# Performance work log

Hardware: AMD Instinct MI355X
Metric: run time of the kernel (lower is better)

Reference implementation:

```python
import jax, jax.numpy as jnp
import numpy as np

B, NPTS = 2, 60000
NX, NY = 256, 256
PCR0, PCR1 = -32.0, -32.0
PS0, PS1 = 0.25, 0.25
MAXPP = 32      # max points per pillar
MAXP = 12000    # max pillars
C = 64          # lidar_channels
SENT = NX * NY  # sentinel pillar id (> any valid id)
NEG = -1e9
EPS = 1e-5


def setup_inputs():
    key = jax.random.key(0)
    ks = jax.random.split(key, 16)
    xy = jax.random.uniform(ks[0], (B, NPTS, 2), minval=-34.0, maxval=34.0)
    z = jax.random.uniform(ks[1], (B, NPTS, 1), minval=-3.0, maxval=1.0)
    ir = jax.random.uniform(ks[2], (B, NPTS, 2))
    pts = jnp.concatenate([xy, z, ir], axis=-1).astype(jnp.float32)
    mask = jax.random.uniform(ks[3], (B, NPTS)) < 0.98

    def lin(k, i, o):
        return (jax.random.normal(k, (i, o)) / np.sqrt(i)).astype(jnp.float32)

    inp = {"lidar_points": pts, "lidar_mask": mask,
           "w1": lin(ks[4], 10, 64), "b1": 0.01 * jax.random.normal(ks[5], (64,), jnp.float32),
           "g1": jnp.ones(64, jnp.float32), "be1": jnp.zeros(64, jnp.float32),
           "w2": lin(ks[6], 64, 64), "b2": 0.01 * jax.random.normal(ks[7], (64,), jnp.float32),
           "g2": jnp.ones(64, jnp.float32), "be2": jnp.zeros(64, jnp.float32)}
    for i, n in enumerate(["1", "2", "3"]):
        inp["cw" + n] = (jax.random.normal(ks[8 + i], (64, 64, 3, 3)) / np.sqrt(64 * 9)).astype(jnp.float32)
        inp["cb" + n] = 0.01 * jax.random.normal(ks[11 + i], (64,), jnp.float32)
        inp["cg" + n] = jnp.ones(64, jnp.float32)
        inp["cbe" + n] = jnp.zeros(64, jnp.float32)
    return inp


def bn1d(x, g, b):  # training-mode BN over rows (biased var), matches torch BatchNorm1d forward
    m = x.mean(0)
    v = ((x - m) ** 2).mean(0)
    return (x - m) * jax.lax.rsqrt(v + EPS) * g + b


def bn2d(x, g, b):  # training-mode BN over (N,H,W) per channel
    m = x.mean((0, 2, 3), keepdims=True)
    v = ((x - m) ** 2).mean((0, 2, 3), keepdims=True)
    return (x - m) * jax.lax.rsqrt(v + EPS) * g[None, :, None, None] + b[None, :, None, None]


def conv3(x, w, b):
    y = jax.lax.conv_general_dilated(x, w, (1, 1), 'SAME',
                                     dimension_numbers=('NCHW', 'OIHW', 'NCHW'))
    return y + b[None, :, None, None]


def pillarize(pts, msk):
    """pts: (N,5) xyzir, msk: (N,) bool -> padded pillar tensors (fixed shapes)."""
    n = pts.shape[0]
    ix = jnp.clip(((pts[:, 0] - PCR0) / PS0).astype(jnp.int32), 0, NX - 1)
    iy = jnp.clip(((pts[:, 1] - PCR1) / PS1).astype(jnp.int32), 0, NY - 1)
    pid = jnp.where(msk, iy * NX + ix, SENT)
    # sorted unique ids; keep the first (smallest) MAXP, like torch.unique + truncation
    spid = jnp.sort(pid)
    is_new = jnp.concatenate([jnp.array([True]), spid[1:] != spid[:-1]])
    urank = jnp.cumsum(is_new) - 1
    dest = jnp.where(is_new & (urank < MAXP) & (spid < SENT), urank, MAXP)
    uids = jnp.full((MAXP + 1,), SENT, dtype=pid.dtype).at[dest].set(spid)[:MAXP]  # ascending, SENT-padded
    inv = jnp.clip(jnp.searchsorted(uids, pid), 0, MAXP - 1)
    valid = (uids[inv] == pid) & (pid < SENT)
    # rank of each point within its pillar, in original point order (stable sort)
    seg = jnp.where(valid, inv, MAXP)
    order = jnp.argsort(seg)  # stable
    sseg = seg[order]
    pos = jnp.arange(n)
    first = jnp.concatenate([jnp.array([True]), sseg[1:] != sseg[:-1]])
    start = jax.lax.cummax(jnp.where(first, pos, 0))
    rank = jnp.zeros(n, jnp.int32).at[order].set((pos - start).astype(jnp.int32))
    keep = valid & (rank < MAXPP)  # first MAXPP points per pillar (matches truncation-then-mean)
    seg2 = jnp.where(keep, inv, MAXP)  # dump slot = MAXP
    cnt = jnp.zeros(MAXP + 1, pts.dtype).at[seg2].add(1.0)
    sums = jnp.zeros((MAXP + 1, 3), pts.dtype).at[seg2].add(jnp.where(keep[:, None], pts[:, :3], 0.0))
    mean = sums / jnp.maximum(cnt, 1.0)[:, None]
    ctr = mean[seg2]  # per-point pillar centroid (over kept points)
    gx = PCR0 + ((pid % NX).astype(pts.dtype) + 0.5) * PS0
    gy = PCR1 + ((pid // NX).astype(pts.dtype) + 0.5) * PS1
    aug = jnp.concatenate([pts, pts[:, :3] - ctr, gx[:, None], gy[:, None]], axis=1)  # (N,10)
    rk = jnp.minimum(rank, MAXPP - 1)
    pf = jnp.zeros((MAXP + 1, MAXPP, 10), pts.dtype).at[seg2, rk].set(
        jnp.where(keep[:, None], aug, 0.0))[:MAXP]
    pm = jnp.zeros((MAXP + 1, MAXPP), bool).at[seg2, rk].set(keep)[:MAXP]
    pvalid = uids < SENT
    coords = jnp.where(pvalid[:, None], jnp.stack([uids % NX, uids // NX], axis=-1), 0)
    return pf, pm, coords, pvalid


def pillar_net(pf, pm, w1, b1, g1, be1, w2, b2, g2, be2):
    npil, pp, ci = pf.shape
    x = pf.reshape(npil * pp, ci) @ w1 + b1
    x = jax.nn.relu(bn1d(x, g1, be1))
    x = x @ w2 + b2
    x = jax.nn.relu(bn1d(x, g2, be2))
    x = x.reshape(npil, pp, -1)
    x = jnp.where(pm[:, :, None], x, NEG)
    return x.max(axis=1)  # (npil, C)


def reference(lidar_points, lidar_mask, w1, b1, g1, be1, w2, b2, g2, be2,
              cw1, cb1, cg1, cbe1, cw2, cb2, cg2, cbe2, cw3, cb3, cg3, cbe3):
    pf, pm, coords, pvalid = jax.vmap(pillarize)(lidar_points, lidar_mask)
    # pillar net is applied per batch element in the original loop -> per-sample BN stats
    feat = jax.vmap(lambda a, m: pillar_net(a, m, w1, b1, g1, be1, w2, b2, g2, be2))(pf, pm)
    lin = coords[..., 1] * NX + coords[..., 0]          # (B, MAXP)
    f = jnp.where(pvalid[..., None], feat, 0.0)          # padded pillars contribute nothing
    bev = jax.vmap(lambda l, ff: jnp.zeros((NY * NX, C), ff.dtype).at[l].add(ff))(lin, f)
    bev = bev.reshape(-1, NY, NX, C).transpose(0, 3, 1, 2)  # (B,C,NY,NX)
    x = jax.nn.relu(bn2d(conv3(bev, cw1, cb1), cg1, cbe1))
    x = jax.nn.relu(bn2d(conv3(x, cw2, cb2), cg2, cbe2))
    x = jax.nn.relu(bn2d(conv3(x, cw3, cb3), cg3, cbe3))
    return x
```

## Files before the change

kernel.cpp:

```cpp
#include <hip/hip_runtime.h>

#define NPTS 60000
#define NXG 256
#define NCELL 65536
#define MAXP 12000
#define MAXPP 32
#define NROWS (MAXP*MAXPP)

typedef float f32x32 __attribute__((ext_vector_type(32)));
typedef float f32x4  __attribute__((ext_vector_type(4)));
typedef short s16x8  __attribute__((ext_vector_type(8)));

__device__ __forceinline__ short to_bf16(float f){
  unsigned u = __float_as_uint(f);
  unsigned r = (u + 0x7FFFu + ((u>>16)&1u)) >> 16;
  return (short)r;
}

__global__ __launch_bounds__(256) void zero_bufs(uint4* __restrict__ p1, size_t n1,
                                                 uint4* __restrict__ p2, size_t n2){
  size_t idx = (size_t)blockIdx.x*256 + threadIdx.x;
  size_t stride = (size_t)gridDim.x*256;
  const uint4 z = make_uint4(0,0,0,0);
  for (size_t k=idx; k<n1; k+=stride) p1[k]=z;
  for (size_t k=idx; k<n2; k+=stride) p2[k]=z;
}

__global__ void compute_pid(const float* __restrict__ pts, const void* __restrict__ maskp,
                            int* __restrict__ pid, int* __restrict__ pptr,
                            int* __restrict__ ccnt){
  __shared__ int cf32, cbig;
  if (threadIdx.x==0){ cf32=0; cbig=0; }
  __syncthreads();
  {
    int lf=0, lb=0;
    const unsigned* mu = (const unsigned*)maskp;
    for (int k=0;k<4;k++){
      unsigned x = mu[threadIdx.x*4+k];
      if (x==0x3f800000u) lf++;
      else if (x>1u) lb++;
    }
    if (lf) atomicAdd(&cf32, lf);
    if (lb) atomicAdd(&cbig, lb);
  }
  __syncthreads();
  int mode = (cf32>64) ? 2 : ((cbig>0) ? 1 : 0);
  int i = blockIdx.x*blockDim.x + threadIdx.x;
  if (i>=NPTS) return;
  int b = blockIdx.y;
  int gi = b*NPTS+i;
  bool m;
  if (mode==0)      m = ((const int*)maskp)[gi]!=0;
  else if (mode==1) m = ((const unsigned char*)maskp)[gi]!=0;
  else              m = ((const float*)maskp)[gi]!=0.f;
  int cell = -1;
  if (m){
    float x = pts[(size_t)gi*5+0], y = pts[(size_t)gi*5+1];
    int ix = (int)((x - (-32.0f)) / 0.25f);
    ix = ix<0?0:(ix>255?255:ix);
    int iy = (int)((y - (-32.0f)) / 0.25f);
    iy = iy<0?0:(iy>255?255:iy);
    cell = iy*NXG + ix;
    atomicAdd(&ccnt[b*NCELL+cell], 1);
  }
  pid[gi] = cell;
  pptr[gi] = -1;
}

__global__ __launch_bounds__(256) void scan_a(const int* __restrict__ ccnt,
                                              int2* __restrict__ bpart){
  int b = blockIdx.y, blk = blockIdx.x, t = threadIdx.x;
  int4 v = *(const int4*)&ccnt[b*NCELL + blk*1024 + t*4];
  int occ = (v.x>0)+(v.y>0)+(v.z>0)+(v.w>0);
  int cnt = v.x+v.y+v.z+v.w;
  #pragma unroll
  for (int off=32; off>0; off>>=1){
    occ += __shfl_xor(occ, off, 64);
    cnt += __shfl_xor(cnt, off, 64);
  }
  __shared__ int so[4], sc[4];
  int wv = t>>6, lane = t&63;
  if (lane==0){ so[wv]=occ; sc[wv]=cnt; }
  __syncthreads();
  if (t==0) bpart[b*64+blk] = make_int2(so[0]+so[1]+so[2]+so[3], sc[0]+sc[1]+sc[2]+sc[3]);
}

__global__ __launch_bounds__(256) void scan_b(const int* __restrict__ ccnt,
    const int2* __restrict__ bpart,
    int* __restrict__ crank, int* __restrict__ cstart, int* __restrict__ pcell,
    int* __restrict__ misc, int* __restrict__ heavy){
  __shared__ int swo[4], swc[4], sk[4];
  __shared__ int bo_, bc_;
  int b = blockIdx.y, blk = blockIdx.x, t = threadIdx.x;
  int wv = t>>6, lane = t&63;
  if (t < 64){
    int2 p = bpart[b*64+t];
    int po = (t<blk)? p.x : 0;
    int pc = (t<blk)? p.y : 0;
    int to = p.x;
    int tc = p.y;
    #pragma unroll
    for (int off=32; off>0; off>>=1){
      po += __shfl_xor(po, off, 64);
      pc += __shfl_xor(pc, off, 64);
      to += __shfl_xor(to, off, 64);
      tc += __shfl_xor(tc, off, 64);
    }
    if (t==0){
      bo_ = po; bc_ = pc;
      if (blk==0){
        misc[1+b] = (to < MAXP) ? to : MAXP;
        misc[5+b] = tc;
      }
    }
  }
  int4 v = *(const int4*)&ccnt[b*NCELL + blk*1024 + t*4];
  int occ = (v.x>0)+(v.y>0)+(v.z>0)+(v.w>0);
  int cnt = v.x+v.y+v.z+v.w;
  int io = occ, ic = cnt;
  #pragma unroll
  for (int off=1; off<64; off<<=1){
    int ao = __shfl_up(io, off, 64);
    int ac = __shfl_up(ic, off, 64);
    if (lane >= off){ io += ao; ic += ac; }
  }
  if (lane==63){ swo[wv]=io; swc[wv]=ic; }
  __syncthreads();
  int wvo=0, wvc=0;
  #pragma unroll
  for (int w2=0; w2<4; w2++){
    if (w2<wv){ wvo += swo[w2]; wvc += swc[w2]; }
  }
  int eo = bo_ + wvo + io - occ;
  int ec = bc_ + wvc + ic - cnt;
  int kept = 0;
  int cellb = blk*1024 + t*4;
  int vv[4] = {v.x,v.y,v.z,v.w};
  #pragma unroll
  for (int j=0;j<4;j++){
    int c = cellb+j; int val = vv[j];
    if (val>0){
      crank[b*NCELL+c]=eo; cstart[b*NCELL+c]=ec;
      if (eo<MAXP){
        pcell[b*MAXP+eo]=c;
        kept += (val<MAXPP)? val : MAXPP;
        if (val>MAXPP){
          int hi = atomicAdd(&heavy[b],1);
          if (hi<64) heavy[2 + b*64 + hi] = c;
        }
      }
      eo++; ec+=val;
    }
  }
  #pragma unroll
  for (int off=32; off>0; off>>=1) kept += __shfl_xor(kept, off, 64);
  if (lane==0) sk[wv]=kept;
  __syncthreads();
  if (t==0) atomicAdd(&misc[3+b], sk[0]+sk[1]+sk[2]+sk[3]);
}

__global__ void scatter_points(const int* __restrict__ pid, const int* __restrict__ ccnt,
    const int* __restrict__ crank, const int* __restrict__ cstart,
    int* __restrict__ ctmp, int* __restrict__ plist, int* __restrict__ pptr){
  int i = blockIdx.x*blockDim.x + threadIdx.x;
  if (i>=NPTS) return;
  int b = blockIdx.y;
  int gi = b*NPTS+i;
  int cell = pid[gi];
  if (cell<0) return;
  int bc = b*NCELL+cell;
  int pos = cstart[bc] + atomicAdd(&ctmp[bc],1);
  plist[b*NPTS+pos] = i;
  int r = crank[bc];
  if (r>=0 && r<MAXP && ccnt[bc]<=MAXPP) pptr[gi] = r;
}

__global__ void heavy_select(const int* __restrict__ ccnt, const int* __restrict__ crank,
    const int* __restrict__ cstart, const int* __restrict__ plist,
    const int* __restrict__ heavy, int* __restrict__ pptr){
  int b = blockIdx.y;
  int hn = heavy[b]; if (hn>64) hn=64;
  if ((int)blockIdx.x >= hn) return;
  int cell = heavy[2 + b*64 + blockIdx.x];
  int bc = b*NCELL+cell;
  int cnt = ccnt[bc], start = cstart[bc], pr = crank[bc];
  for (int e=threadIdx.x; e<cnt; e+=blockDim.x){
    int pe = plist[b*NPTS+start+e];
    int rank=0;
    for (int k=0;k<cnt;k++) rank += (plist[b*NPTS+start+k] < pe);
    if (rank<MAXPP) pptr[b*NPTS+pe] = pr;
  }
}

__global__ __launch_bounds__(256) void gather_cpts(const float* __restrict__ pts,
    const int* __restrict__ pid, const int* __restrict__ pptr,
    const int* __restrict__ plist, const int* __restrict__ misc,
    float* __restrict__ cpts, float* __restrict__ psum){
  int pos = blockIdx.x*256 + threadIdx.x;
  int b = blockIdx.y;
  if (pos >= misc[5+b]) return;
  int i = plist[b*NPTS+pos];
  int gi = b*NPTS+i;
  const float* qp = &pts[(size_t)gi*5];
  float x=qp[0], y=qp[1], z=qp[2], i1=qp[3], i2=qp[4];
  int cell = pid[gi];
  int rid = pptr[gi];
  float gx = -32.0f + ((float)(cell&255)+0.5f)*0.25f;
  float gy = -32.0f + ((float)(cell>>8)+0.5f)*0.25f;
  float4* cp = (float4*)&cpts[(size_t)(b*NPTS+pos)*8];
  cp[0] = make_float4(x,y,z,i1);
  cp[1] = make_float4(i2,gx,gy,__int_as_float(rid));
  if (rid>=0){
    float* s = &psum[(size_t)(b*MAXP+rid)*4];
    atomicAdd(s+0,x); atomicAdd(s+1,y); atomicAdd(s+2,z); atomicAdd(s+3,1.f);
  }
}

#define MM_ACC(K,V) { if ((K)<32) m0[(K)&31]+=(V); else if ((K)<64) m1[((K)-32)&31]+=(V); else m2+=(V); }
__global__ __launch_bounds__(256) void moments(const float* __restrict__ cpts,
    const float* __restrict__ psum, const int* __restrict__ misc,
    float* __restrict__ lstat){
  int b = blockIdx.y;
  int n = misc[5+b];
  f32x32 m0, m1; float m2 = 0.f;
  #pragma unroll
  for (int j=0;j<32;j++){ m0[j]=0.f; m1[j]=0.f; }
  for (int pos = blockIdx.x*256+threadIdx.x; pos<n; pos += gridDim.x*256){
    const float4* cp = (const float4*)&cpts[(size_t)(b*NPTS+pos)*8];
    float4 f1 = cp[0], f2 = cp[1];
    int rid = __float_as_int(f2.w);
    if (rid<0) continue;
    float4 mc = *(const float4*)&psum[(size_t)(b*MAXP+rid)*4];
    float inv = 1.f/fmaxf(mc.w,1.f);
    float aug[10] = {f1.x,f1.y,f1.z,f1.w,f2.x,
                     f1.x-mc.x*inv, f1.y-mc.y*inv, f1.z-mc.z*inv, f2.y, f2.z};
    #pragma unroll
    for (int d=0; d<10; d++){
      #pragma unroll
      for (int e=d; e<10; e++){
        const int k = d*10 - d*(d-1)/2 + (e-d);
        MM_ACC(k, aug[d]*aug[e]);
      }
      const int kl = 55+d;
      MM_ACC(kl, aug[d]);
    }
  }
  int lane = threadIdx.x & 63;
  int rep = ((blockIdx.x*256+threadIdx.x)>>6) & 15;
  float* dst = &lstat[(size_t)(rep*2+b)*65];
  #pragma unroll
  for (int j=0;j<32;j++){
    float v = m0[j];
    #pragma unroll
    for (int off=32; off>0; off>>=1) v += __shfl_xor(v, off, 64);
    if (lane==0) atomicAdd(&dst[j], v);
  }
  #pragma unroll
  for (int j=0;j<32;j++){
    float v = m1[j];
    #pragma unroll
    for (int off=32; off>0; off>>=1) v += __shfl_xor(v, off, 64);
    if (lane==0) atomicAdd(&dst[32+j], v);
  }
  {
    float v = m2;
    #pragma unroll
    for (int off=32; off>0; off>>=1) v += __shfl_xor(v, off, 64);
    if (lane==0) atomicAdd(&dst[64], v);
  }
}

__global__ void stats_fin1(const float* __restrict__ w1, const float* __restrict__ b1,
    const float* __restrict__ g1, const float* __restrict__ be1,
    const float* __restrict__ w2, const float* __restrict__ b2,
    const float* __restrict__ lstat, float* __restrict__ stats,
    const int* __restrict__ misc){
  __shared__ float M[65];
  __shared__ float z0s[64];
  int b = blockIdx.x, c = threadIdx.x;
  for (int e=c; e<65; e+=64){
    float s=0.f;
    for (int r=0;r<16;r++) s += lstat[(size_t)(r*2+b)*65+e];
    M[e]=s;
  }
  __syncthreads();
  float* S = &stats[(size_t)b*512];
  float wcol[10];
  #pragma unroll
  for (int d=0;d<10;d++) wcol[d] = w1[d*64+c];
  float b1c = b1[c];
  float nk = (float)misc[3+b];
  const float N = (float)NROWS;
  float pad = N - nk;
  float lw = 0.f;
  #pragma unroll
  for (int d=0;d<10;d++) lw += M[55+d]*wcol[d];
  float s = nk*b1c + lw;
  float qq = nk*b1c*b1c + 2.f*b1c*lw;
  #pragma unroll
  for (int d=0; d<10; d++){
    #pragma unroll
    for (int e=d; e<10; e++){
      float m = M[d*10 - d*(d-1)/2 + (e-d)];
      qq += ((d==e)?1.f:2.f)*m*wcol[d]*wcol[e];
    }
  }
  float St = s + pad*b1c;
  float Qt = qq + pad*b1c*b1c;
  float mu = St/N;
  float var = fmaxf(Qt/N - mu*mu, 0.f);
  float sc = g1[c]*rsqrtf(var+1e-5f);
  float sh = be1[c]-mu*sc;
  S[256+c]=sc; S[320+c]=sh;
  float z0 = fmaxf(b1c*sc+sh, 0.f);
  z0s[c]=z0;
  __syncthreads();
  float t0 = b2[c];
  for (int i2=0;i2<64;i2++) t0 += z0s[i2]*w2[(size_t)i2*64+c];
  S[128+c]=pad*t0; S[192+c]=pad*t0*t0;
}

__global__ __launch_bounds__(256) void pillar_mlp(const float* __restrict__ cpts,
    const int* __restrict__ pcell, const int* __restrict__ cstart,
    const int* __restrict__ ccnt, const float* __restrict__ psum,
    const int* __restrict__ misc,
    const float* __restrict__ w1, const float* __restrict__ b1,
    const float* __restrict__ w2, const float* __restrict__ b2,
    const float* __restrict__ stats, float* __restrict__ l2stat,
    float* __restrict__ fmx, float* __restrict__ fmn){
  const int lane = threadIdx.x & 63;
  float w1c[10];
  #pragma unroll
  for (int d=0;d<10;d++) w1c[d] = w1[d*64+lane];
  f32x32 w2lo, w2hi;
  #pragma unroll
  for (int c=0;c<32;c++) w2lo[c] = w2[(size_t)c*64+lane];
  #pragma unroll
  for (int c=0;c<32;c++) w2hi[c] = w2[(size_t)(c+32)*64+lane];
  const float b1c = b1[lane], b2c = b2[lane];
  const float sc1_0 = stats[256+lane], sh1_0 = stats[320+lane];
  const float sc1_1 = stats[512+256+lane], sh1_1 = stats[512+320+lane];
  const int npil0 = misc[1], npil1 = misc[2];
  float s2_0=0.f, q2_0=0.f, s2_1=0.f, q2_1=0.f;

  const int wglobal = (blockIdx.x*256 + threadIdx.x) >> 6;
  const int nwaves = (gridDim.x*256) >> 6;
  for (int qq = wglobal; qq < 2*MAXP; qq += nwaves){
    int b = (qq >= MAXP) ? 1 : 0;
    int p = qq - b*MAXP;
    int npil = b ? npil1 : npil0;
    if (p >= npil) continue;
    int cell = pcell[b*MAXP+p];
    int bc = b*NCELL+cell;
    int cnt = ccnt[bc], start = cstart[bc];
    const float* mc = &psum[(size_t)(b*MAXP+p)*4];
    float minv = 1.f/fmaxf(mc[3],1.f);
    float mx = mc[0]*minv, my = mc[1]*minv, mz = mc[2]*minv;
    float gx = -32.0f + ((float)(cell&255)+0.5f)*0.25f;
    float gy = -32.0f + ((float)(cell>>8)+0.5f)*0.25f;
    float sc1 = b ? sc1_1 : sc1_0;
    float sh1 = b ? sh1_1 : sh1_0;
    float tmax = -1e30f, tmin = 1e30f;
    float s2 = 0.f, q2 = 0.f;
    for (int k=0; k<cnt; k++){
      const float4* cp = (const float4*)&cpts[(size_t)(b*NPTS+start+k)*8];
      float4 f1 = cp[0], f2 = cp[1];
      int rid = __float_as_int(f2.w);
      if (rid != p) continue;
      float x=f1.x, y=f1.y, z=f1.z, i1=f1.w, i2=f2.x;
      float acc = b1c;
      acc = fmaf(x, w1c[0], acc);
      acc = fmaf(y, w1c[1], acc);
      acc = fmaf(z, w1c[2], acc);
      acc = fmaf(i1, w1c[3], acc);
      acc = fmaf(i2, w1c[4], acc);
      acc = fmaf(x-mx, w1c[5], acc);
      acc = fmaf(y-my, w1c[6], acc);
      acc = fmaf(z-mz, w1c[7], acc);
      acc = fmaf(gx, w1c[8], acc);
      acc = fmaf(gy, w1c[9], acc);
      float zz = fmaxf(acc*sc1+sh1, 0.f);
      float t = b2c;
      #pragma unroll
      for (int c=0;c<32;c++){
        float zc = __int_as_float(__builtin_amdgcn_readlane(__float_as_int(zz), c));
        t = fmaf(zc, w2lo[c], t);
      }
      #pragma unroll
      for (int c=0;c<32;c++){
        float zc = __int_as_float(__builtin_amdgcn_readlane(__float_as_int(zz), c+32));
        t = fmaf(zc, w2hi[c], t);
      }
      tmax = fmaxf(tmax, t);
      tmin = fminf(tmin, t);
      s2 += t; q2 += t*t;
    }
    fmx[(size_t)(b*MAXP+p)*64 + lane] = tmax;
    fmn[(size_t)(b*MAXP+p)*64 + lane] = tmin;
    if (b){ s2_1 += s2; q2_1 += q2; } else { s2_0 += s2; q2_0 += q2; }
  }
  int rep = wglobal & 15;
  atomicAdd(&l2stat[((rep*2+0)*2+0)*64+lane], s2_0);
  atomicAdd(&l2stat[((rep*2+0)*2+1)*64+lane], q2_0);
  atomicAdd(&l2stat[((rep*2+1)*2+0)*64+lane], s2_1);
  atomicAdd(&l2stat[((rep*2+1)*2+1)*64+lane], q2_1);
}

__global__ void stats_fin2(const float* __restrict__ g2,const float* __restrict__ be2,
                           const float* __restrict__ l2stat, float* __restrict__ stats){
  int b = blockIdx.x, c = threadIdx.x;
  float* S = &stats[(size_t)b*512];
  float s = S[128+c], q = S[192+c];
  for (int r=0;r<16;r++){
    s += l2stat[((r*2+b)*2+0)*64+c];
    q += l2stat[((r*2+b)*2+1)*64+c];
  }
  const float N = (float)NROWS;
  float m = s/N;
  float v = fmaxf(q/N - m*m, 0.f);
  float sc = g2[c]*rsqrtf(v+1e-5f);
  S[384+c]=sc; S[448+c]=be2[c]-m*sc;
}

__global__ void scatter_bev(const float* __restrict__ fmx, const float* __restrict__ fmn,
                            const int* __restrict__ pcell, const int* __restrict__ misc,
                            const float* __restrict__ stats, short* __restrict__ bevh){
  int tid = blockIdx.x*256+threadIdx.x;
  if (tid >= 2*64*MAXP) return;
  int c = tid & 63;
  int bp = tid >> 6;
  int b = bp / MAXP;
  int p = bp - b*MAXP;
  if (p >= misc[1+b]) return;
  float sc2 = stats[(size_t)b*512+384+c], sh2 = stats[(size_t)b*512+448+c];
  float t = (sc2 >= 0.f) ? fmx[tid] : fmn[tid];
  float v = fmaxf(sc2*t+sh2, 0.f);
  int cell = pcell[b*MAXP+p];
  bevh[((size_t)((b<<16) + cell))*64 + c] = to_bf16(v);
}

__global__ void wcvt3(const float* __restrict__ w0, const float* __restrict__ w1,
                      const float* __restrict__ w2, short* __restrict__ wh){
  int t = blockIdx.x*256 + threadIdx.x;
  if (t >= 3*36864) return;
  int l = t / 36864, r = t - l*36864;
  const float* w = (l==0)? w0 : ((l==1)? w1 : w2);
  int ic = r & 63, oc = (r>>6)&63, tap = r>>12;
  wh[t] = to_bf16(w[(oc*64+ic)*9 + tap]);
}

#define MFMA16(A,B,C) __builtin_amdgcn_mfma_f32_16x16x32_bf16(A,B,C,0,0,0)

__global__ __launch_bounds__(256,3) void conv_mfma(const short* __restrict__ xh,
    const short* __restrict__ wh, const float* __restrict__ bias,
    const float* __restrict__ pstat, const float* __restrict__ pg, const float* __restrict__ pbe,
    short* __restrict__ outh, float* __restrict__ outf,
    float* __restrict__ stat){
  __shared__ short sX[18*18*40];
  __shared__ short sW[288*40];
  __shared__ float sBN[128];
  __shared__ float ss[32], sq[32];
  const int tX = blockIdx.x*16, tY = blockIdx.y*16;
  const int b = blockIdx.z >> 1, ocbase = (blockIdx.z & 1)*32;
  const int t = threadIdx.x;
  const int lane = t & 63, wv = t >> 6;
  const int colx = lane & 15;
  const int kb = (lane >> 4) * 8;
  if (t < 32){ ss[t]=0.f; sq[t]=0.f; }
  if (t < 64 && pstat){
    const float n = 131072.f;
    float m = pstat[t]/n;
    float v = fmaxf(pstat[64+t]/n - m*m, 0.f);
    float sc = pg[t]*rsqrtf(v+1e-5f);
    sBN[t]=sc; sBN[64+t]=pbe[t]-m*sc;
  }

  f32x4 a00={0.f,0.f,0.f,0.f}, a01=a00, a02=a00, a03=a00;
  f32x4 a10=a00, a11=a00, a12=a00, a13=a00;

  for (int h=0; h<2; ++h){
    __syncthreads();
    for (int e=t; e<1296; e+=256){
      int px = e>>2, j = e&3;
      int yy = px/18, xx = px - yy*18;
      int gy = tY+yy-1, gx = tX+xx-1;
      uint4 v = make_uint4(0,0,0,0);
      if ((unsigned)gy<256u && (unsigned)gx<256u){
        v = *(const uint4*)&xh[((size_t)((b<<16) + (gy<<8) + gx))*64 + h*32 + j*8];
        if (pstat){
          unsigned arr[4] = {v.x, v.y, v.z, v.w};
          #pragma unroll
          for (int j2=0;j2<4;j2++){
            unsigned wrd = arr[j2];
            int ch = h*32 + j*8 + j2*2;
            float lo = __uint_as_float(wrd<<16);
            float hi = __uint_as_float(wrd & 0xffff0000u);
            lo = fmaxf(lo*sBN[ch]+sBN[64+ch], 0.f);
            hi = fmaxf(hi*sBN[ch+1]+sBN[64+ch+1], 0.f);
            arr[j2] = (unsigned)(unsigned short)to_bf16(lo) |
                      (((unsigned)(unsigned short)to_bf16(hi))<<16);
          }
          v = make_uint4(arr[0],arr[1],arr[2],arr[3]);
        }
      }
      *(uint4*)&sX[px*40 + j*8] = v;
    }
    for (int e=t; e<1152; e+=256){
      int row = e>>2, j = e&3;
      int tap = row>>5, ocl = row&31;
      uint4 v = *(const uint4*)&wh[(size_t)tap*4096 + (ocbase+ocl)*64 + h*32 + j*8];
      *(uint4*)&sW[row*40 + j*8] = v;
    }
    __syncthreads();
    #pragma unroll
    for (int tap=0; tap<9; ++tap){
      const int dy = tap/3, dx = tap - dy*3;
      s16x8 wA = *(const s16x8*)&sW[(tap*32 +  0 + colx)*40 + kb];
      s16x8 wB = *(const s16x8*)&sW[(tap*32 + 16 + colx)*40 + kb];
      s16x8 x0 = *(const s16x8*)&sX[((wv*4+0+dy)*18 + colx+dx)*40 + kb];
      s16x8 x1 = *(const s16x8*)&sX[((wv*4+1+dy)*18 + colx+dx)*40 + kb];
      s16x8 x2 = *(const s16x8*)&sX[((wv*4+2+dy)*18 + colx+dx)*40 + kb];
      s16x8 x3 = *(const s16x8*)&sX[((wv*4+3+dy)*18 + colx+dx)*40 + kb];
      a00 = MFMA16(wA,x0,a00); a01 = MFMA16(wA,x1,a01);
      a02 = MFMA16(wA,x2,a02); a03 = MFMA16(wA,x3,a03);
      a10 = MFMA16(wB,x0,a10); a11 = MFMA16(wB,x1,a11);
      a12 = MFMA16(wB,x2,a12); a13 = MFMA16(wB,x3,a13);
    }
  }
  const int ocl = (lane>>4)*4;
  #define DOG(G, A0,A1,A2,A3) { \
    const int lc = G*16 + ocl; \
    const int oc0g = ocbase + lc; \
    float bj0=bias[oc0g], bj1=bias[oc0g+1], bj2=bias[oc0g+2], bj3=bias[oc0g+3]; \
    float v00=A0[0]+bj0, v01=A0[1]+bj1, v02=A0[2]+bj2, v03=A0[3]+bj3; \
    float v10=A1[0]+bj0, v11=A1[1]+bj1, v12=A1[2]+bj2, v13=A1[3]+bj3; \
    float v20=A2[0]+bj0, v21=A2[1]+bj1, v22=A2[2]+bj2, v23=A2[3]+bj3; \
    float v30=A3[0]+bj0, v31=A3[1]+bj1, v32=A3[2]+bj2, v33=A3[3]+bj3; \
    float s0=v00+v10+v20+v30, q0=v00*v00+v10*v10+v20*v20+v30*v30; \
    float s1=v01+v11+v21+v31, q1=v01*v01+v11*v11+v21*v21+v31*v31; \
    float s2=v02+v12+v22+v32, q2=v02*v02+v12*v12+v22*v22+v32*v32; \
    float s3=v03+v13+v23+v33, q3=v03*v03+v13*v13+v23*v23+v33*v33; \
    s0+=__shfl_xor(s0,1,64); s0+=__shfl_xor(s0,2,64); s0+=__shfl_xor(s0,4,64); s0+=__shfl_xor(s0,8,64); \
    q0+=__shfl_xor(q0,1,64); q0+=__shfl_xor(q0,2,64); q0+=__shfl_xor(q0,4,64); q0+=__shfl_xor(q0,8,64); \
    s1+=__shfl_xor(s1,1,64); s1+=__shfl_xor(s1,2,64); s1+=__shfl_xor(s1,4,64); s1+=__shfl_xor(s1,8,64); \
    q1+=__shfl_xor(q1,1,64); q1+=__shfl_xor(q1,2,64); q1+=__shfl_xor(q1,4,64); q1+=__shfl_xor(q1,8,64); \
    s2+=__shfl_xor(s2,1,64); s2+=__shfl_xor(s2,2,64); s2+=__shfl_xor(s2,4,64); s2+=__shfl_xor(s2,8,64); \
    q2+=__shfl_xor(q2,1,64); q2+=__shfl_xor(q2,2,64); q2+=__shfl_xor(q2,4,64); q2+=__shfl_xor(q2,8,64); \
    s3+=__shfl_xor(s3,1,64); s3+=__shfl_xor(s3,2,64); s3+=__shfl_xor(s3,4,64); s3+=__shfl_xor(s3,8,64); \
    q3+=__shfl_xor(q3,1,64); q3+=__shfl_xor(q3,2,64); q3+=__shfl_xor(q3,4,64); q3+=__shfl_xor(q3,8,64); \
    if (colx==0){ \
      atomicAdd(&ss[lc],s0);   atomicAdd(&sq[lc],q0); \
      atomicAdd(&ss[lc+1],s1); atomicAdd(&sq[lc+1],q1); \
      atomicAdd(&ss[lc+2],s2); atomicAdd(&sq[lc+2],q2); \
      atomicAdd(&ss[lc+3],s3); atomicAdd(&sq[lc+3],q3); \
    } \
    if (outh){ \
      size_t pb = (size_t)((b<<16) + tX + colx); \
      *(short4*)&outh[(pb + ((tY+wv*4+0)<<8))*64 + oc0g] = make_short4(to_bf16(v00),to_bf16(v01),to_bf16(v02),to_bf16(v03)); \
      *(short4*)&outh[(pb + ((tY+wv*4+1)<<8))*64 + oc0g] = make_short4(to_bf16(v10),to_bf16(v11),to_bf16(v12),to_bf16(v13)); \
      *(short4*)&outh[(pb + ((tY+wv*4+2)<<8))*64 + oc0g] = make_short4(to_bf16(v20),to_bf16(v21),to_bf16(v22),to_bf16(v23)); \
      *(short4*)&outh[(pb + ((tY+wv*4+3)<<8))*64 + oc0g] = make_short4(to_bf16(v30),to_bf16(v31),to_bf16(v32),to_bf16(v33)); \
    } else { \
      size_t cb0 = (((size_t)(b*64+oc0g))<<16) + ((tY+wv*4)<<8) + tX + colx; \
      outf[cb0          ] = v00; outf[cb0+(1<<16)      ] = v01; outf[cb0+(2<<16)      ] = v02; outf[cb0+(3<<16)      ] = v03; \
      outf[cb0+256      ] = v10; outf[cb0+(1<<16)+256  ] = v11; outf[cb0+(2<<16)+256  ] = v12; outf[cb0+(3<<16)+256  ] = v13; \
      outf[cb0+512      ] = v20; outf[cb0+(1<<16)+512  ] = v21; outf[cb0+(2<<16)+512  ] = v22; outf[cb0+(3<<16)+512  ] = v23; \
      outf[cb0+768      ] = v30; outf[cb0+(1<<16)+768  ] = v31; outf[cb0+(2<<16)+768  ] = v32; outf[cb0+(3<<16)+768  ] = v33; \
    } \
  }
  DOG(0, a00,a01,a02,a03)
  DOG(1, a10,a11,a12,a13)
  #undef DOG
  __syncthreads();
  if (t < 32){
    atomicAdd(&stat[ocbase+t],    ss[t]);
    atomicAdd(&stat[64+ocbase+t], sq[t]);
  }
}

__global__ __launch_bounds__(256) void bn_apply(float* __restrict__ x, const float* __restrict__ bnst,
                                                const float* __restrict__ g, const float* __restrict__ be){
  __shared__ float sBN[128];
  if (threadIdx.x < 64){
    int c = threadIdx.x;
    const float n = 131072.f;
    float m = bnst[c]/n;
    float v = fmaxf(bnst[64+c]/n - m*m, 0.f);
    float sc = g[c]*rsqrtf(v+1e-5f);
    sBN[c]=sc; sBN[64+c]=be[c]-m*sc;
  }
  __syncthreads();
  size_t idx = (size_t)blockIdx.x*256 + threadIdx.x;
  size_t stride = (size_t)gridDim.x*256;
  float4* p = (float4*)x;
  for (size_t k=idx; k<2097152ULL; k+=stride){
    int c = (int)((k>>14)&63);
    float sc = sBN[c], sh = sBN[64+c];
    float4 v = p[k];
    v.x=fmaxf(v.x*sc+sh,0.f); v.y=fmaxf(v.y*sc+sh,0.f);
    v.z=fmaxf(v.z*sc+sh,0.f); v.w=fmaxf(v.w*sc+sh,0.f);
    p[k]=v;
  }
}

extern "C" void kernel_launch(void* const* d_in, const int* in_sizes, int n_in,
                              void* d_out, int out_size, void* d_ws, size_t ws_size,
                              hipStream_t stream){
  const float* pts  = (const float*)d_in[0];
  const void*  mask = d_in[1];
  const float* w1 = (const float*)d_in[2];
  const float* b1 = (const float*)d_in[3];
  const float* g1 = (const float*)d_in[4];
  const float* be1= (const float*)d_in[5];
  const float* w2 = (const float*)d_in[6];
  const float* b2 = (const float*)d_in[7];
  const float* g2 = (const float*)d_in[8];
  const float* be2= (const float*)d_in[9];
  const float* cw[3]  = {(const float*)d_in[10],(const float*)d_in[14],(const float*)d_in[18]};
  const float* cb[3]  = {(const float*)d_in[11],(const float*)d_in[15],(const float*)d_in[19]};
  const float* cg[3]  = {(const float*)d_in[12],(const float*)d_in[16],(const float*)d_in[20]};
  const float* cbe[3] = {(const float*)d_in[13],(const float*)d_in[17],(const float*)d_in[21]};
  float* out = (float*)d_out;

  char* W = (char*)d_ws;
  size_t off = 0;
  auto A = [&](size_t n){ size_t r = off; off = (off + n + 255) & ~(size_t)255; return r; };
  short*    BIGH  = (short*)   (W + A((size_t)2*NCELL*64*2));
  short*    OUT1H = (short*)   (W + A((size_t)2*NCELL*64*2));
  int*      PID   = (int*)     (W + A((size_t)2*NPTS*4));
  int*      CRANK = (int*)     (W + A((size_t)2*NCELL*4));
  int*      CSTART= (int*)     (W + A((size_t)2*NCELL*4));
  int*      PLIST = (int*)     (W + A((size_t)2*NPTS*4));
  int*      PPTR  = (int*)     (W + A((size_t)2*NPTS*4));
  int*      PCELL = (int*)     (W + A((size_t)2*MAXP*4));
  float*    CPTS  = (float*)   (W + A((size_t)2*NPTS*8*4));
  float*    FMX   = (float*)   (W + A((size_t)2*MAXP*64*4));
  float*    FMN   = (float*)   (W + A((size_t)2*MAXP*64*4));
  short*    WH    = (short*)   (W + A((size_t)3*36864*2));
  int2*     BPART = (int2*)    (W + A((size_t)2*64*8));
  size_t zbeg = off;
  int*      CCNT  = (int*)     (W + A((size_t)2*NCELL*4));
  int*      CTMP  = (int*)     (W + A((size_t)2*NCELL*4));
  float*    PSUM  = (float*)   (W + A((size_t)2*MAXP*16));
  float*    STATS = (float*)   (W + A((size_t)2*512*4));
  float*    LSTAT = (float*)   (W + A((size_t)16*2*65*4));
  float*    L2STAT= (float*)   (W + A((size_t)16*2*2*64*4));
  float*    BNST  = (float*)   (W + A((size_t)3*256*4));
  int*      HEAVY = (int*)     (W + A((size_t)(2+2*64)*4));
  int*      MISC  = (int*)     (W + A(256));
  size_t zend = off;

  zero_bufs<<<2048,256,0,stream>>>((uint4*)BIGH, (size_t)2*NCELL*64*2/16,
                                   (uint4*)(W+zbeg), (zend-zbeg)/16);

  dim3 perPt((NPTS+255)/256, 2);

  compute_pid<<<perPt,256,0,stream>>>(pts, mask, PID, PPTR, CCNT);
  wcvt3<<<432,256,0,stream>>>(cw[0], cw[1], cw[2], WH);
  scan_a<<<dim3(64,2),256,0,stream>>>(CCNT, BPART);
  scan_b<<<dim3(64,2),256,0,stream>>>(CCNT, BPART, CRANK, CSTART, PCELL, MISC, HEAVY);
  scatter_points<<<perPt,256,0,stream>>>(PID, CCNT, CRANK, CSTART, CTMP, PLIST, PPTR);
  heavy_select<<<dim3(64,2),64,0,stream>>>(CCNT, CRANK, CSTART, PLIST, HEAVY, PPTR);
  gather_cpts<<<perPt,256,0,stream>>>(pts, PID, PPTR, PLIST, MISC, CPTS, PSUM);
  moments<<<dim3(120,2),256,0,stream>>>(CPTS, PSUM, MISC, LSTAT);
  stats_fin1<<<2,64,0,stream>>>(w1, b1, g1, be1, w2, b2, LSTAT, STATS, MISC);
  pillar_mlp<<<2048,256,0,stream>>>(CPTS, PCELL, CSTART, CCNT, PSUM, MISC,
                                    w1, b1, w2, b2, STATS, L2STAT, FMX, FMN);
  stats_fin2<<<2,64,0,stream>>>(g2, be2, L2STAT, STATS);
  scatter_bev<<<(2*64*MAXP+255)/256,256,0,stream>>>(FMX, FMN, PCELL, MISC, STATS, BIGH);

  conv_mfma<<<dim3(16,16,4),256,0,stream>>>(BIGH, WH, cb[0], nullptr, nullptr, nullptr,
                                            OUT1H, nullptr, BNST);
  conv_mfma<<<dim3(16,16,4),256,0,stream>>>(OUT1H, WH+36864, cb[1], BNST, cg[0], cbe[0],
                                            BIGH, nullptr, BNST+256);
  conv_mfma<<<dim3(16,16,4),256,0,stream>>>(BIGH, WH+2*36864, cb[2], BNST+256, cg[1], cbe[1],
                                            nullptr, out, BNST+512);
  bn_apply<<<2048,256,0,stream>>>(out, BNST+512, cg[2], cbe[2]);
}
```

Measured before the change: 237.0 us.

## Merge setup kernels and compute all 64 output channels per conv block

The weight conversion is folded into the zeroing kernel. The BN1 statistics finalisation is moved into pillar_mlp, with each block recomputing it, and into stats_fin2, which removes two small launches. The conv kernel now uses 512-thread blocks that each cover all 64 output channels for one 16x16 tile. This halves the grid and removes the duplicate loading of the input halo tile that happened when two blocks split the output channels. In exchange, shared-memory weight staging doubles and every pillar_mlp block redundantly reduces the lstat partials.

```diff
diff --git a/kernel.cpp b/kernel.cpp
--- a/kernel.cpp
+++ b/kernel.cpp
@@ -17,13 +17,21 @@
   return (short)r;
 }
 
-__global__ __launch_bounds__(256) void zero_bufs(uint4* __restrict__ p1, size_t n1,
-                                                 uint4* __restrict__ p2, size_t n2){
+__global__ __launch_bounds__(256) void prep(uint4* __restrict__ p1, size_t n1,
+                                            uint4* __restrict__ p2, size_t n2,
+                                            const float* __restrict__ w0, const float* __restrict__ w1,
+                                            const float* __restrict__ w2, short* __restrict__ wh){
   size_t idx = (size_t)blockIdx.x*256 + threadIdx.x;
   size_t stride = (size_t)gridDim.x*256;
   const uint4 z = make_uint4(0,0,0,0);
   for (size_t k=idx; k<n1; k+=stride) p1[k]=z;
   for (size_t k=idx; k<n2; k+=stride) p2[k]=z;
+  for (size_t k=idx; k<3*36864; k+=stride){
+    int l = (int)(k / 36864), r = (int)(k - (size_t)l*36864);
+    const float* w = (l==0)? w0 : ((l==1)? w1 : w2);
+    int ic = r & 63, oc = (r>>6)&63, tap = r>>12;
+    wh[k] = to_bf16(w[(oc*64+ic)*9 + tap]);
+  }
 }
 
 __global__ void compute_pid(const float* __restrict__ pts, const void* __restrict__ maskp,
@@ -270,76 +278,61 @@
   }
 }
 
-__global__ void stats_fin1(const float* __restrict__ w1, const float* __restrict__ b1,
-    const float* __restrict__ g1, const float* __restrict__ be1,
-    const float* __restrict__ w2, const float* __restrict__ b2,
-    const float* __restrict__ lstat, float* __restrict__ stats,
-    const int* __restrict__ misc){
-  __shared__ float M[65];
-  __shared__ float z0s[64];
-  int b = blockIdx.x, c = threadIdx.x;
-  for (int e=c; e<65; e+=64){
-    float s=0.f;
-    for (int r=0;r<16;r++) s += lstat[(size_t)(r*2+b)*65+e];
-    M[e]=s;
-  }
-  __syncthreads();
-  float* S = &stats[(size_t)b*512];
-  float wcol[10];
-  #pragma unroll
-  for (int d=0;d<10;d++) wcol[d] = w1[d*64+c];
-  float b1c = b1[c];
-  float nk = (float)misc[3+b];
-  const float N = (float)NROWS;
-  float pad = N - nk;
-  float lw = 0.f;
-  #pragma unroll
-  for (int d=0;d<10;d++) lw += M[55+d]*wcol[d];
-  float s = nk*b1c + lw;
-  float qq = nk*b1c*b1c + 2.f*b1c*lw;
-  #pragma unroll
-  for (int d=0; d<10; d++){
-    #pragma unroll
-    for (int e=d; e<10; e++){
-      float m = M[d*10 - d*(d-1)/2 + (e-d)];
-      qq += ((d==e)?1.f:2.f)*m*wcol[d]*wcol[e];
-    }
-  }
-  float St = s + pad*b1c;
-  float Qt = qq + pad*b1c*b1c;
-  float mu = St/N;
-  float var = fmaxf(Qt/N - mu*mu, 0.f);
-  float sc = g1[c]*rsqrtf(var+1e-5f);
-  float sh = be1[c]-mu*sc;
-  S[256+c]=sc; S[320+c]=sh;
-  float z0 = fmaxf(b1c*sc+sh, 0.f);
-  z0s[c]=z0;
-  __syncthreads();
-  float t0 = b2[c];
-  for (int i2=0;i2<64;i2++) t0 += z0s[i2]*w2[(size_t)i2*64+c];
-  S[128+c]=pad*t0; S[192+c]=pad*t0*t0;
-}
-
 __global__ __launch_bounds__(256) void pillar_mlp(const float* __restrict__ cpts,
     const int* __restrict__ pcell, const int* __restrict__ cstart,
     const int* __restrict__ ccnt, const float* __restrict__ psum,
     const int* __restrict__ misc,
     const float* __restrict__ w1, const float* __restrict__ b1,
+    const float* __restrict__ g1, const float* __restrict__ be1,
     const float* __restrict__ w2, const float* __restrict__ b2,
-    const float* __restrict__ stats, float* __restrict__ l2stat,
+    const float* __restrict__ lstat, float* __restrict__ l2stat,
     float* __restrict__ fmx, float* __restrict__ fmn){
+  __shared__ float sM[2][65];
   const int lane = threadIdx.x & 63;
   float w1c[10];
   #pragma unroll
   for (int d=0;d<10;d++) w1c[d] = w1[d*64+lane];
+  for (int e=threadIdx.x; e<130; e+=256){
+    int bb = e/65, k = e-bb*65;
+    float s=0.f;
+    for (int r=0;r<16;r++) s += lstat[(size_t)(r*2+bb)*65+k];
+    sM[bb][k]=s;
+  }
+  __syncthreads();
+  const float b1c = b1[lane], b2c = b2[lane];
+  const float g1c = g1[lane], be1c = be1[lane];
+  float sc1_0, sh1_0, sc1_1, sh1_1;
+  #pragma unroll
+  for (int bb=0;bb<2;bb++){
+    float nk = (float)misc[3+bb];
+    const float N = (float)NROWS;
+    float pad = N - nk;
+    float lw = 0.f;
+    #pragma unroll
+    for (int d=0;d<10;d++) lw += sM[bb][55+d]*w1c[d];
+    float s = nk*b1c + lw;
+    float qq = nk*b1c*b1c + 2.f*b1c*lw;
+    #pragma unroll
+    for (int d=0; d<10; d++){
+      #pragma unroll
+      for (int e=d; e<10; e++){
+        float m = sM[bb][d*10 - d*(d-1)/2 + (e-d)];
+        qq += ((d==e)?1.f:2.f)*m*w1c[d]*w1c[e];
+      }
+    }
+    float St = s + pad*b1c;
+    float Qt = qq + pad*b1c*b1c;
+    float mu = St/N;
+    float var = fmaxf(Qt/N - mu*mu, 0.f);
+    float sc = g1c*rsqrtf(var+1e-5f);
+    float sh = be1c-mu*sc;
+    if (bb){ sc1_1=sc; sh1_1=sh; } else { sc1_0=sc; sh1_0=sh; }
+  }
   f32x32 w2lo, w2hi;
   #pragma unroll
   for (int c=0;c<32;c++) w2lo[c] = w2[(size_t)c*64+lane];
   #pragma unroll
   for (int c=0;c<32;c++) w2hi[c] = w2[(size_t)(c+32)*64+lane];
-  const float b1c = b1[lane], b2c = b2[lane];
-  const float sc1_0 = stats[256+lane], sh1_0 = stats[320+lane];
-  const float sc1_1 = stats[512+256+lane], sh1_1 = stats[512+320+lane];
   const int npil0 = misc[1], npil1 = misc[2];
   float s2_0=0.f, q2_0=0.f, s2_1=0.f, q2_1=0.f;
 
@@ -406,20 +399,62 @@
   atomicAdd(&l2stat[((rep*2+1)*2+1)*64+lane], q2_1);
 }
 
-__global__ void stats_fin2(const float* __restrict__ g2,const float* __restrict__ be2,
-                           const float* __restrict__ l2stat, float* __restrict__ stats){
+__global__ void stats_fin2(const float* __restrict__ w1, const float* __restrict__ b1,
+    const float* __restrict__ g1, const float* __restrict__ be1,
+    const float* __restrict__ w2, const float* __restrict__ b2,
+    const float* __restrict__ g2, const float* __restrict__ be2,
+    const float* __restrict__ lstat, const float* __restrict__ l2stat,
+    const int* __restrict__ misc, float* __restrict__ stats){
+  __shared__ float M[65];
+  __shared__ float z0s[64];
   int b = blockIdx.x, c = threadIdx.x;
+  for (int e=c; e<65; e+=64){
+    float s=0.f;
+    for (int r=0;r<16;r++) s += lstat[(size_t)(r*2+b)*65+e];
+    M[e]=s;
+  }
+  __syncthreads();
+  float wcol[10];
+  #pragma unroll
+  for (int d=0;d<10;d++) wcol[d] = w1[d*64+c];
+  float b1c = b1[c];
+  float nk = (float)misc[3+b];
+  const float N = (float)NROWS;
+  float pad = N - nk;
+  float lw = 0.f;
+  #pragma unroll
+  for (int d=0;d<10;d++) lw += M[55+d]*wcol[d];
+  float s = nk*b1c + lw;
+  float qq = nk*b1c*b1c + 2.f*b1c*lw;
+  #pragma unroll
+  for (int d=0; d<10; d++){
+    #pragma unroll
+    for (int e=d; e<10; e++){
+      float m = M[d*10 - d*(d-1)/2 + (e-d)];
+      qq += ((d==e)?1.f:2.f)*m*wcol[d]*wcol[e];
+    }
+  }
+  float St = s + pad*b1c;
+  float Qt = qq + pad*b1c*b1c;
+  float mu = St/N;
+  float var = fmaxf(Qt/N - mu*mu, 0.f);
+  float sc1 = g1[c]*rsqrtf(var+1e-5f);
+  float sh1 = be1[c]-mu*sc1;
+  float z0 = fmaxf(b1c*sc1+sh1, 0.f);
+  z0s[c]=z0;
+  __syncthreads();
+  float t0 = b2[c];
+  for (int i2=0;i2<64;i2++) t0 += z0s[i2]*w2[(size_t)i2*64+c];
+  float s2 = pad*t0, q2 = pad*t0*t0;
+  for (int r=0;r<16;r++){
+    s2 += l2stat[((r*2+b)*2+0)*64+c];
+    q2 += l2stat[((r*2+b)*2+1)*64+c];
+  }
+  float m2 = s2/N;
+  float v2 = fmaxf(q2/N - m2*m2, 0.f);
+  float sc2 = g2[c]*rsqrtf(v2+1e-5f);
   float* S = &stats[(size_t)b*512];
-  float s = S[128+c], q = S[192+c];
-  for (int r=0;r<16;r++){
-    s += l2stat[((r*2+b)*2+0)*64+c];
-    q += l2stat[((r*2+b)*2+1)*64+c];
-  }
-  const float N = (float)NROWS;
-  float m = s/N;
-  float v = fmaxf(q/N - m*m, 0.f);
-  float sc = g2[c]*rsqrtf(v+1e-5f);
-  S[384+c]=sc; S[448+c]=be2[c]-m*sc;
+  S[384+c]=sc2; S[448+c]=be2[c]-m2*sc2;
 }
 
 __global__ void scatter_bev(const float* __restrict__ fmx, const float* __restrict__ fmn,
@@ -439,40 +474,33 @@
   bevh[((size_t)((b<<16) + cell))*64 + c] = to_bf16(v);
 }
 
-__global__ void wcvt3(const float* __restrict__ w0, const float* __restrict__ w1,
-                      const float* __restrict__ w2, short* __restrict__ wh){
-  int t = blockIdx.x*256 + threadIdx.x;
-  if (t >= 3*36864) return;
-  int l = t / 36864, r = t - l*36864;
-  const float* w = (l==0)? w0 : ((l==1)? w1 : w2);
-  int ic = r & 63, oc = (r>>6)&63, tap = r>>12;
-  wh[t] = to_bf16(w[(oc*64+ic)*9 + tap]);
-}
-
 #define MFMA16(A,B,C) __builtin_amdgcn_mfma_f32_16x16x32_bf16(A,B,C,0,0,0)
 
-__global__ __launch_bounds__(256,3) void conv_mfma(const short* __restrict__ xh,
+__global__ __launch_bounds__(512,4) void conv_mfma(const short* __restrict__ xh,
     const short* __restrict__ wh, const float* __restrict__ bias,
     const float* __restrict__ pstat, const float* __restrict__ pg, const float* __restrict__ pbe,
     short* __restrict__ outh, float* __restrict__ outf,
     float* __restrict__ stat){
-  __shared__ short sX[18*18*40];
-  __shared__ short sW[288*40];
+  __shared__ short sX[324*40];
+  __shared__ short sW[576*40];
   __shared__ float sBN[128];
-  __shared__ float ss[32], sq[32];
+  __shared__ float ss[64], sq[64];
   const int tX = blockIdx.x*16, tY = blockIdx.y*16;
-  const int b = blockIdx.z >> 1, ocbase = (blockIdx.z & 1)*32;
+  const int b = blockIdx.z;
   const int t = threadIdx.x;
   const int lane = t & 63, wv = t >> 6;
   const int colx = lane & 15;
   const int kb = (lane >> 4) * 8;
-  if (t < 32){ ss[t]=0.f; sq[t]=0.f; }
-  if (t < 64 && pstat){
+  const int ocb = (wv >> 2) * 32;
+  const int ry  = (wv & 3) * 4;
+  if (t < 64){ ss[t]=0.f; sq[t]=0.f; }
+  if (t >= 64 && t < 128 && pstat){
+    int c = t-64;
     const float n = 131072.f;
-    float m = pstat[t]/n;
-    float v = fmaxf(pstat[64+t]/n - m*m, 0.f);
-    float sc = pg[t]*rsqrtf(v+1e-5f);
-    sBN[t]=sc; sBN[64+t]=pbe[t]-m*sc;
+    float m = pstat[c]/n;
+    float v = fmaxf(pstat[64+c]/n - m*m, 0.f);
+    float sc = pg[c]*rsqrtf(v+1e-5f);
+    sBN[c]=sc; sBN[64+c]=pbe[c]-m*sc;
   }
 
   f32x4 a00={0.f,0.f,0.f,0.f}, a01=a00, a02=a00, a03=a00;
@@ -480,7 +508,7 @@
 
   for (int h=0; h<2; ++h){
     __syncthreads();
-    for (int e=t; e<1296; e+=256){
+    for (int e=t; e<1296; e+=512){
       int px = e>>2, j = e&3;
       int yy = px/18, xx = px - yy*18;
       int gy = tY+yy-1, gx = tX+xx-1;
@@ -505,22 +533,22 @@
       }
       *(uint4*)&sX[px*40 + j*8] = v;
     }
-    for (int e=t; e<1152; e+=256){
+    for (int e=t; e<2304; e+=512){
       int row = e>>2, j = e&3;
-      int tap = row>>5, ocl = row&31;
-      uint4 v = *(const uint4*)&wh[(size_t)tap*4096 + (ocbase+ocl)*64 + h*32 + j*8];
+      int tap = row>>6, oc = row&63;
+      uint4 v = *(const uint4*)&wh[(size_t)tap*4096 + oc*64 + h*32 + j*8];
       *(uint4*)&sW[row*40 + j*8] = v;
     }
     __syncthreads();
     #pragma unroll
     for (int tap=0; tap<9; ++tap){
       const int dy = tap/3, dx = tap - dy*3;
-      s16x8 wA = *(const s16x8*)&sW[(tap*32 +  0 + colx)*40 + kb];
-      s16x8 wB = *(const s16x8*)&sW[(tap*32 + 16 + colx)*40 + kb];
-      s16x8 x0 = *(const s16x8*)&sX[((wv*4+0+dy)*18 + colx+dx)*40 + kb];
-      s16x8 x1 = *(const s16x8*)&sX[((wv*4+1+dy)*18 + colx+dx)*40 + kb];
-      s16x8 x2 = *(const s16x8*)&sX[((wv*4+2+dy)*18 + colx+dx)*40 + kb];
-      s16x8 x3 = *(const s16x8*)&sX[((wv*4+3+dy)*18 + colx+dx)*40 + kb];
+      s16x8 wA = *(const s16x8*)&sW[(tap*64 + ocb +  0 + colx)*40 + kb];
+      s16x8 wB = *(const s16x8*)&sW[(tap*64 + ocb + 16 + colx)*40 + kb];
+      s16x8 x0 = *(const s16x8*)&sX[((ry+0+dy)*18 + colx+dx)*40 + kb];
+      s16x8 x1 = *(const s16x8*)&sX[((ry+1+dy)*18 + colx+dx)*40 + kb];
+      s16x8 x2 = *(const s16x8*)&sX[((ry+2+dy)*18 + colx+dx)*40 + kb];
+      s16x8 x3 = *(const s16x8*)&sX[((ry+3+dy)*18 + colx+dx)*40 + kb];
       a00 = MFMA16(wA,x0,a00); a01 = MFMA16(wA,x1,a01);
       a02 = MFMA16(wA,x2,a02); a03 = MFMA16(wA,x3,a03);
       a10 = MFMA16(wB,x0,a10); a11 = MFMA16(wB,x1,a11);
@@ -529,8 +557,7 @@
   }
   const int ocl = (lane>>4)*4;
   #define DOG(G, A0,A1,A2,A3) { \
-    const int lc = G*16 + ocl; \
-    const int oc0g = ocbase + lc; \
+    const int oc0g = ocb + G*16 + ocl; \
     float bj0=bias[oc0g], bj1=bias[oc0g+1], bj2=bias[oc0g+2], bj3=bias[oc0g+3]; \
     float v00=A0[0]+bj0, v01=A0[1]+bj1, v02=A0[2]+bj2, v03=A0[3]+bj3; \
     float v10=A1[0]+bj0, v11=A1[1]+bj1, v12=A1[2]+bj2, v13=A1[3]+bj3; \
@@ -549,19 +576,19 @@
     s3+=__shfl_xor(s3,1,64); s3+=__shfl_xor(s3,2,64); s3+=__shfl_xor(s3,4,64); s3+=__shfl_xor(s3,8,64); \
     q3+=__shfl_xor(q3,1,64); q3+=__shfl_xor(q3,2,64); q3+=__shfl_xor(q3,4,64); q3+=__shfl_xor(q3,8,64); \
     if (colx==0){ \
-      atomicAdd(&ss[lc],s0);   atomicAdd(&sq[lc],q0); \
-      atomicAdd(&ss[lc+1],s1); atomicAdd(&sq[lc+1],q1); \
-      atomicAdd(&ss[lc+2],s2); atomicAdd(&sq[lc+2],q2); \
-      atomicAdd(&ss[lc+3],s3); atomicAdd(&sq[lc+3],q3); \
+      atomicAdd(&ss[oc0g],s0);   atomicAdd(&sq[oc0g],q0); \
+      atomicAdd(&ss[oc0g+1],s1); atomicAdd(&sq[oc0g+1],q1); \
+      atomicAdd(&ss[oc0g+2],s2); atomicAdd(&sq[oc0g+2],q2); \
+      atomicAdd(&ss[oc0g+3],s3); atomicAdd(&sq[oc0g+3],q3); \
     } \
     if (outh){ \
       size_t pb = (size_t)((b<<16) + tX + colx); \
-      *(short4*)&outh[(pb + ((tY+wv*4+0)<<8))*64 + oc0g] = make_short4(to_bf16(v00),to_bf16(v01),to_bf16(v02),to_bf16(v03)); \
-      *(short4*)&outh[(pb + ((tY+wv*4+1)<<8))*64 + oc0g] = make_short4(to_bf16(v10),to_bf16(v11),to_bf16(v12),to_bf16(v13)); \
-      *(short4*)&outh[(pb + ((tY+wv*4+2)<<8))*64 + oc0g] = make_short4(to_bf16(v20),to_bf16(v21),to_bf16(v22),to_bf16(v23)); \
-      *(short4*)&outh[(pb + ((tY+wv*4+3)<<8))*64 + oc0g] = make_short4(to_bf16(v30),to_bf16(v31),to_bf16(v32),to_bf16(v33)); \
+      *(short4*)&outh[(pb + ((tY+ry+0)<<8))*64 + oc0g] = make_short4(to_bf16(v00),to_bf16(v01),to_bf16(v02),to_bf16(v03)); \
+      *(short4*)&outh[(pb + ((tY+ry+1)<<8))*64 + oc0g] = make_short4(to_bf16(v10),to_bf16(v11),to_bf16(v12),to_bf16(v13)); \
+      *(short4*)&outh[(pb + ((tY+ry+2)<<8))*64 + oc0g] = make_short4(to_bf16(v20),to_bf16(v21),to_bf16(v22),to_bf16(v23)); \
+      *(short4*)&outh[(pb + ((tY+ry+3)<<8))*64 + oc0g] = make_short4(to_bf16(v30),to_bf16(v31),to_bf16(v32),to_bf16(v33)); \
     } else { \
-      size_t cb0 = (((size_t)(b*64+oc0g))<<16) + ((tY+wv*4)<<8) + tX + colx; \
+      size_t cb0 = (((size_t)(b*64+oc0g))<<16) + ((tY+ry)<<8) + tX + colx; \
       outf[cb0          ] = v00; outf[cb0+(1<<16)      ] = v01; outf[cb0+(2<<16)      ] = v02; outf[cb0+(3<<16)      ] = v03; \
       outf[cb0+256      ] = v10; outf[cb0+(1<<16)+256  ] = v11; outf[cb0+(2<<16)+256  ] = v12; outf[cb0+(3<<16)+256  ] = v13; \
       outf[cb0+512      ] = v20; outf[cb0+(1<<16)+512  ] = v21; outf[cb0+(2<<16)+512  ] = v22; outf[cb0+(3<<16)+512  ] = v23; \
@@ -572,9 +599,9 @@
   DOG(1, a10,a11,a12,a13)
   #undef DOG
   __syncthreads();
-  if (t < 32){
-    atomicAdd(&stat[ocbase+t],    ss[t]);
-    atomicAdd(&stat[64+ocbase+t], sq[t]);
+  if (t < 64){
+    atomicAdd(&stat[t],    ss[t]);
+    atomicAdd(&stat[64+t], sq[t]);
   }
 }
 
@@ -650,30 +677,29 @@
   int*      MISC  = (int*)     (W + A(256));
   size_t zend = off;
 
-  zero_bufs<<<2048,256,0,stream>>>((uint4*)BIGH, (size_t)2*NCELL*64*2/16,
-                                   (uint4*)(W+zbeg), (zend-zbeg)/16);
+  prep<<<2048,256,0,stream>>>((uint4*)BIGH, (size_t)2*NCELL*64*2/16,
+                              (uint4*)(W+zbeg), (zend-zbeg)/16,
+                              cw[0], cw[1], cw[2], WH);
 
   dim3 perPt((NPTS+255)/256, 2);
 
   compute_pid<<<perPt,256,0,stream>>>(pts, mask, PID, PPTR, CCNT);
-  wcvt3<<<432,256,0,stream>>>(cw[0], cw[1], cw[2], WH);
   scan_a<<<dim3(64,2),256,0,stream>>>(CCNT, BPART);
   scan_b<<<dim3(64,2),256,0,stream>>>(CCNT, BPART, CRANK, CSTART, PCELL, MISC, HEAVY);
   scatter_points<<<perPt,256,0,stream>>>(PID, CCNT, CRANK, CSTART, CTMP, PLIST, PPTR);
   heavy_select<<<dim3(64,2),64,0,stream>>>(CCNT, CRANK, CSTART, PLIST, HEAVY, PPTR);
   gather_cpts<<<perPt,256,0,stream>>>(pts, PID, PPTR, PLIST, MISC, CPTS, PSUM);
   moments<<<dim3(120,2),256,0,stream>>>(CPTS, PSUM, MISC, LSTAT);
-  stats_fin1<<<2,64,0,stream>>>(w1, b1, g1, be1, w2, b2, LSTAT, STATS, MISC);
   pillar_mlp<<<2048,256,0,stream>>>(CPTS, PCELL, CSTART, CCNT, PSUM, MISC,
-                                    w1, b1, w2, b2, STATS, L2STAT, FMX, FMN);
-  stats_fin2<<<2,64,0,stream>>>(g2, be2, L2STAT, STATS);
+                                    w1, b1, g1, be1, w2, b2, LSTAT, L2STAT, FMX, FMN);
+  stats_fin2<<<2,64,0,stream>>>(w1, b1, g1, be1, w2, b2, g2, be2, LSTAT, L2STAT, MISC, STATS);
   scatter_bev<<<(2*64*MAXP+255)/256,256,0,stream>>>(FMX, FMN, PCELL, MISC, STATS, BIGH);
 
-  conv_mfma<<<dim3(16,16,4),256,0,stream>>>(BIGH, WH, cb[0], nullptr, nullptr, nullptr,
+  conv_mfma<<<dim3(16,16,2),512,0,stream>>>(BIGH, WH, cb[0], nullptr, nullptr, nullptr,
                                             OUT1H, nullptr, BNST);
-  conv_mfma<<<dim3(16,16,4),256,0,stream>>>(OUT1H, WH+36864, cb[1], BNST, cg[0], cbe[0],
+  conv_mfma<<<dim3(16,16,2),512,0,stream>>>(OUT1H, WH+36864, cb[1], BNST, cg[0], cbe[0],
                                             BIGH, nullptr, BNST+256);
-  conv_mfma<<<dim3(16,16,4),256,0,stream>>>(BIGH, WH+2*36864, cb[2], BNST+256, cg[1], cbe[1],
+  conv_mfma<<<dim3(16,16,2),512,0,stream>>>(BIGH, WH+2*36864, cb[2], BNST+256, cg[1], cbe[1],
                                             nullptr, out, BNST+512);
   bn_apply<<<2048,256,0,stream>>>(out, BNST+512, cg[2], cbe[2]);
 }
```

Measured after the change: 220.3 us. 7.0% less time.
